# Kernel optimization log

Hardware: AMD Instinct MI355X
Metric: run time of the kernel (lower is better)

The kernel has to match this reference:

```python
import jax, jax.numpy as jnp
import numpy as np

B, S, HID = 2, 2048, 4096
NH, NKV, D = 32, 8, 128  # heads, kv heads, head_dim
GROUPS = NH // NKV
THETA = 10000.0


def _rope_tables():
    inv_freq = 1.0 / (THETA ** (np.arange(0, D, 2, dtype=np.float32) / D))
    pos = np.arange(S, dtype=np.float32)
    freqs = pos[:, None] * inv_freq[None, :]          # [S, D/2]
    emb = np.concatenate([freqs, freqs], axis=-1)      # [S, D]
    cos = np.broadcast_to(np.cos(emb)[None], (B, S, D)).copy()
    sin = np.broadcast_to(np.sin(emb)[None], (B, S, D)).copy()
    return jnp.asarray(cos), jnp.asarray(sin)


def setup_inputs() -> dict:
    key = jax.random.key(0)
    ks = jax.random.split(key, 5)
    hidden_states = jax.random.normal(ks[0], (B, S, HID), dtype=jnp.float32)
    cos, sin = _rope_tables()
    std = 0.02
    Wq = jax.random.normal(ks[1], (NH * D, HID), dtype=jnp.float32) * std
    Wk = jax.random.normal(ks[2], (NKV * D, HID), dtype=jnp.float32) * std
    Wv = jax.random.normal(ks[3], (NKV * D, HID), dtype=jnp.float32) * std
    Wo = jax.random.normal(ks[4], (HID, NH * D), dtype=jnp.float32) * std
    return {"hidden_states": hidden_states, "cos": cos, "sin": sin,
            "Wq": Wq, "Wk": Wk, "Wv": Wv, "Wo": Wo}


def _rotate_half(x):
    x1, x2 = jnp.split(x, 2, axis=-1)
    return jnp.concatenate([-x2, x1], axis=-1)


def reference(hidden_states, cos, sin, Wq, Wk, Wv, Wo):
    b, s, _ = hidden_states.shape
    # QKV projections (no bias; attention_bias=False)
    q = (hidden_states @ Wq.T).reshape(b, s, NH, D).transpose(0, 2, 1, 3)    # [B,NH,S,D]
    k = (hidden_states @ Wk.T).reshape(b, s, NKV, D).transpose(0, 2, 1, 3)   # [B,NKV,S,D]
    v = (hidden_states @ Wv.T).reshape(b, s, NKV, D).transpose(0, 2, 1, 3)
    # RoPE (HF apply_rotary_pos_emb: cos/sin unsqueezed at head dim)
    c = cos[:, None, :, :]
    sn = sin[:, None, :, :]
    q = q * c + _rotate_half(q) * sn
    k = k * c + _rotate_half(k) * sn
    # GQA repeat_kv
    k = jnp.repeat(k, GROUPS, axis=1)                                        # [B,NH,S,D]
    v = jnp.repeat(v, GROUPS, axis=1)
    # dense evalmode: scores + causal mask + fp32 softmax
    scores = jnp.einsum('bhqd,bhkd->bhqk', q, k) / jnp.sqrt(jnp.float32(D))
    causal = jnp.triu(jnp.ones((s, s), dtype=bool), k=1)                     # True above diag
    scores = jnp.where(causal[None, None], jnp.float32(-jnp.inf), scores)
    attn = jax.nn.softmax(scores.astype(jnp.float32), axis=-1).astype(v.dtype)
    out = jnp.einsum('bhqk,bhkd->bhqd', attn, v)                             # [B,NH,S,D]
    out = out.transpose(0, 2, 1, 3).reshape(b, s, NH * D)
    return out @ Wo.T
```

## Files before the change

### kernel.cpp

```cpp
#include <hip/hip_runtime.h>
#include <hip/hip_bf16.h>

#define DEV __device__ __forceinline__

typedef __attribute__((ext_vector_type(8))) short bf16x8;
typedef __attribute__((ext_vector_type(4))) short s16x4;
typedef __attribute__((ext_vector_type(4))) float f32x4;

constexpr int B_ = 2, S_ = 2048, HID_ = 4096, NH_ = 32, NKV_ = 8, D_ = 128;
constexpr int GROUPS_ = NH_ / NKV_;
constexpr float QSCALE_ = 0.08838834764831845f * 1.4426950408889634f;

DEV unsigned short f2bf(float x) {
    union { float f; unsigned int u; } v; v.f = x;
    unsigned int r = v.u + 0x7fffu + ((v.u >> 16) & 1u);
    return (unsigned short)(r >> 16);
}

DEV f32x4 mfma16(bf16x8 a, bf16x8 b, f32x4 c) {
    return __builtin_amdgcn_mfma_f32_16x16x32_bf16(a, b, c, 0, 0, 0);
}

DEV void gll16(const void* g, void* l) {
    __builtin_amdgcn_global_load_lds(
        (const __attribute__((address_space(1))) unsigned int*)g,
        (__attribute__((address_space(3))) unsigned int*)l, 16, 0, 0);
}

DEV int vperm(int s) {
    return (s & ~31) | (((s >> 2) & 3) << 3) | (((s >> 4) & 1) << 2) | (s & 3);
}

__global__ __launch_bounds__(256) void cast_all_k(
    const float* __restrict__ s0, const float* __restrict__ s1,
    const float* __restrict__ s2, const float* __restrict__ s3,
    const float* __restrict__ s4,
    unsigned short* __restrict__ d0, unsigned short* __restrict__ d1,
    unsigned short* __restrict__ d2, unsigned short* __restrict__ d3,
    unsigned short* __restrict__ d4)
{
    int bb = blockIdx.x;
    const float* s; unsigned short* d; int off;
    if      (bb < 8192)  { s = s0; d = d0; off = bb; }
    else if (bb < 16384) { s = s1; d = d1; off = bb - 8192; }
    else if (bb < 18432) { s = s2; d = d2; off = bb - 16384; }
    else if (bb < 20480) { s = s3; d = d3; off = bb - 18432; }
    else                 { s = s4; d = d4; off = bb - 20480; }
    size_t i = ((size_t)off * 256 + threadIdx.x) * 8;
    const f32x4* sp = (const f32x4*)(s + i);
    f32x4 a = sp[0], b = sp[1];
    bf16x8 o;
    o[0] = (short)f2bf(a[0]); o[1] = (short)f2bf(a[1]);
    o[2] = (short)f2bf(a[2]); o[3] = (short)f2bf(a[3]);
    o[4] = (short)f2bf(b[0]); o[5] = (short)f2bf(b[1]);
    o[6] = (short)f2bf(b[2]); o[7] = (short)f2bf(b[3]);
    *(bf16x8*)(d + i) = o;
}

template<int EPI>
__global__ __launch_bounds__(512, 2) void gemm256_k(
    const unsigned short* __restrict__ A, const unsigned short* __restrict__ Bw,
    float* __restrict__ Cf, unsigned short* __restrict__ Qo,
    const float* __restrict__ cosT, const float* __restrict__ sinT,
    int M, int N, int K)
{
    __shared__ __align__(16) unsigned short lds[65536];
    const int tid = threadIdx.x, lane = tid & 63;
    const int w = tid >> 6, wm = w >> 2, wn = w & 3;
    const int la = lane & 15, lb = lane >> 4;

    const int nwg = (int)gridDim.x;
    const int cpx = nwg >> 3;
    const int bid = (int)blockIdx.x;
    const int sw = (bid & 7) * cpx + (bid >> 3);
    const int ntn = N >> 8;
    const int bm = (sw / ntn) << 8, bn = (sw % ntn) << 8;

    const int srow = tid >> 3;
    const int scol8 = (tid & 7) ^ (srow & 7);
    const size_t rK = (size_t)K;
    const unsigned short* gA = A + (size_t)(bm + srow) * rK + scol8 * 8;
    const unsigned short* gB = Bw + (size_t)(bn + srow) * rK + scol8 * 8;

#define STAGE_A_H0(buf, kt) { gll16(gA + (size_t)(kt),            &lds[(buf)*16384 + tid*8]); \
                              gll16(gA + (size_t)(kt) + 128*rK,   &lds[(buf)*16384 + 8192 + tid*8]); }
#define STAGE_A_H1(buf, kt) { gll16(gA + (size_t)(kt) + 64*rK,    &lds[(buf)*16384 + 4096 + tid*8]); \
                              gll16(gA + (size_t)(kt) + 192*rK,   &lds[(buf)*16384 + 12288 + tid*8]); }
#define STAGE_B_H0(buf, kt) { gll16(gB + (size_t)(kt),            &lds[32768 + (buf)*16384 + tid*8]); \
                              gll16(gB + (size_t)(kt) + 64*rK,    &lds[32768 + (buf)*16384 + 4096 + tid*8]); }
#define STAGE_B_H1(buf, kt) { gll16(gB + (size_t)(kt) + 128*rK,   &lds[32768 + (buf)*16384 + 8192 + tid*8]); \
                              gll16(gB + (size_t)(kt) + 192*rK,   &lds[32768 + (buf)*16384 + 12288 + tid*8]); }
#define SB0() __builtin_amdgcn_sched_barrier(0)

    f32x4 acc[8][4];
#pragma unroll
    for (int m = 0; m < 8; ++m)
#pragma unroll
        for (int j = 0; j < 4; ++j) acc[m][j] = f32x4{0.f, 0.f, 0.f, 0.f};

    auto rdA = [&](int buf, int m, int kk) -> bf16x8 {
        int r = wm * 128 + m * 16 + la;
        int slot = (kk * 4 + lb) ^ (la & 7);
        return *(const bf16x8*)&lds[buf * 16384 + r * 64 + slot * 8];
    };
    auto rdB = [&](int buf, int j, int kk) -> bf16x8 {
        int r = (wn + 4 * j) * 16 + la;
        int slot = (kk * 4 + lb) ^ (la & 7);
        return *(const bf16x8*)&lds[32768 + buf * 16384 + r * 64 + slot * 8];
    };

    STAGE_A_H0(0, 0); STAGE_B_H0(0, 0); STAGE_B_H1(0, 0); STAGE_A_H1(0, 0);

    bf16x8 af[4][2], b01[2][2], b23[2][2];
    int cur = 0;
    const int nt = K >> 6;
    for (int t = 0; t < nt; ++t) {
        const bool pre = (t + 1 < nt);
        const int kn = (t + 1) << 6;
        const int nb = cur ^ 1;
        asm volatile("s_waitcnt vmcnt(2)" ::: "memory");
        SB0(); __builtin_amdgcn_s_barrier(); SB0();
#pragma unroll
        for (int m = 0; m < 4; ++m)
#pragma unroll
            for (int kk = 0; kk < 2; ++kk) af[m][kk] = rdA(cur, m, kk);
#pragma unroll
        for (int j = 0; j < 2; ++j)
#pragma unroll
            for (int kk = 0; kk < 2; ++kk) b01[j][kk] = rdB(cur, j, kk);
        if (pre) STAGE_A_H0(nb, kn);
        __builtin_amdgcn_s_setprio(1);
#pragma unroll
        for (int kk = 0; kk < 2; ++kk)
#pragma unroll
            for (int m = 0; m < 4; ++m)
#pragma unroll
                for (int j = 0; j < 2; ++j)
                    acc[m][j] = mfma16(af[m][kk], b01[j][kk], acc[m][j]);
        __builtin_amdgcn_s_setprio(0);
#pragma unroll
        for (int j = 0; j < 2; ++j)
#pragma unroll
            for (int kk = 0; kk < 2; ++kk) b23[j][kk] = rdB(cur, j + 2, kk);
        if (pre) STAGE_B_H0(nb, kn);
        __builtin_amdgcn_s_setprio(1);
#pragma unroll
        for (int kk = 0; kk < 2; ++kk)
#pragma unroll
            for (int m = 0; m < 4; ++m)
#pragma unroll
                for (int j = 0; j < 2; ++j)
                    acc[m][j + 2] = mfma16(af[m][kk], b23[j][kk], acc[m][j + 2]);
        __builtin_amdgcn_s_setprio(0);
        if (pre) { asm volatile("s_waitcnt vmcnt(4)" ::: "memory"); }
        else     { asm volatile("s_waitcnt vmcnt(0)" ::: "memory"); }
        SB0(); __builtin_amdgcn_s_barrier(); SB0();
#pragma unroll
        for (int m = 0; m < 4; ++m)
#pragma unroll
            for (int kk = 0; kk < 2; ++kk) af[m][kk] = rdA(cur, m + 4, kk);
        if (pre) STAGE_B_H1(nb, kn);
        __builtin_amdgcn_s_setprio(1);
#pragma unroll
        for (int kk = 0; kk < 2; ++kk)
#pragma unroll
            for (int m = 0; m < 4; ++m)
#pragma unroll
                for (int j = 0; j < 2; ++j)
                    acc[m + 4][j + 2] = mfma16(af[m][kk], b23[j][kk], acc[m + 4][j + 2]);
        __builtin_amdgcn_s_setprio(0);
        if (pre) STAGE_A_H1(nb, kn);
        __builtin_amdgcn_s_setprio(1);
#pragma unroll
        for (int kk = 0; kk < 2; ++kk)
#pragma unroll
            for (int m = 0; m < 4; ++m)
#pragma unroll
                for (int j = 0; j < 2; ++j)
                    acc[m + 4][j] = mfma16(af[m][kk], b01[j][kk], acc[m + 4][j]);
        __builtin_amdgcn_s_setprio(0);
        cur ^= 1;
    }
#undef STAGE_A_H0
#undef STAGE_A_H1
#undef STAGE_B_H0
#undef STAGE_B_H1

    const int srow0 = bm + wm * 128;
    if constexpr (EPI == 0) {
#pragma unroll
        for (int m = 0; m < 8; ++m)
#pragma unroll
            for (int j = 0; j < 4; ++j) {
                int col = bn + (wn + 4 * j) * 16 + la;
#pragma unroll
                for (int r = 0; r < 4; ++r)
                    Cf[(size_t)(srow0 + m * 16 + lb * 4 + r) * N + col] = acc[m][j][r];
            }
    } else {
        const int hbase = bn >> 7;
        const int d = wn * 16 + la;
#pragma unroll
        for (int m = 0; m < 8; ++m) {
#pragma unroll
            for (int r = 0; r < 4; ++r) {
                int row = srow0 + m * 16 + lb * 4 + r;
                float cv = cosT[(size_t)row * D_ + d];
                float sv = sinT[(size_t)row * D_ + d];
#pragma unroll
                for (int p = 0; p < 2; ++p) {
                    float x1 = acc[m][p * 2 + 0][r], x2 = acc[m][p * 2 + 1][r];
                    unsigned short* o = Qo + (size_t)row * (NH_ * D_) + (hbase + p) * D_ + d;
                    o[0]  = f2bf((x1 * cv - x2 * sv) * QSCALE_);
                    o[64] = f2bf((x2 * cv + x1 * sv) * QSCALE_);
                }
            }
        }
    }
}

__global__ __launch_bounds__(512, 4) void gemm_kv_k(
    const unsigned short* __restrict__ A, const unsigned short* __restrict__ Bw,
    unsigned short* __restrict__ Ko, unsigned short* __restrict__ Vo,
    const float* __restrict__ cosT, const float* __restrict__ sinT,
    int M, int K)
{
    __shared__ __align__(16) unsigned short lds[32768];
    const int tid = threadIdx.x, lane = tid & 63;
    const int w = tid >> 6, wm = w >> 2, wn = w & 3;
    const int la = lane & 15, lb = lane >> 4;

    const int nwg = (int)gridDim.x;
    const int cpx = nwg >> 3;
    const int bid = (int)blockIdx.x;
    const int sw = (bid & 7) * cpx + (bid >> 3);
    const int ntn = 2048 >> 7;
    const int bm = (sw / ntn) << 7, bn = (sw % ntn) << 7;

    const int srow = tid >> 3;
    const int scol8 = (tid & 7) ^ (srow & 7);
    const size_t rK = (size_t)K;
    const unsigned short* gA = A + (size_t)(bm + srow) * rK + scol8 * 8;
    const unsigned short* gB = Bw + (size_t)(bn + srow) * rK + scol8 * 8;

#define KV_STG_A(buf, kt)  { gll16(gA + (size_t)(kt),          &lds[(buf)*8192 + tid*8]); \
                             gll16(gA + (size_t)(kt) + 64*rK,  &lds[(buf)*8192 + 4096 + tid*8]); }
#define KV_STG_B0(buf, kt)   gll16(gB + (size_t)(kt),          &lds[16384 + (buf)*8192 + tid*8])
#define KV_STG_B1(buf, kt)   gll16(gB + (size_t)(kt) + 64*rK,  &lds[16384 + (buf)*8192 + 4096 + tid*8])
#define SB0() __builtin_amdgcn_sched_barrier(0)

    f32x4 acc[4][2];
#pragma unroll
    for (int m = 0; m < 4; ++m)
#pragma unroll
        for (int j = 0; j < 2; ++j) acc[m][j] = f32x4{0.f, 0.f, 0.f, 0.f};

    auto rdA = [&](int buf, int m, int kk) -> bf16x8 {
        int r = wm * 64 + m * 16 + la;
        int slot = (kk * 4 + lb) ^ (la & 7);
        return *(const bf16x8*)&lds[buf * 8192 + r * 64 + slot * 8];
    };
    auto rdB = [&](int buf, int j, int kk) -> bf16x8 {
        int r = (wn + 4 * j) * 16 + la;
        int slot = (kk * 4 + lb) ^ (la & 7);
        return *(const bf16x8*)&lds[16384 + buf * 8192 + r * 64 + slot * 8];
    };

    KV_STG_A(0, 0); KV_STG_B0(0, 0); KV_STG_B1(0, 0);

    bf16x8 af[4][2], bf0[2], bf1[2];
    int cur = 0;
    const int nt = K >> 6;
    for (int t = 0; t < nt; ++t) {
        const bool pre = (t + 1 < nt);
        const int kn = (t + 1) << 6;
        const int nb = cur ^ 1;
        asm volatile("s_waitcnt vmcnt(1)" ::: "memory");
        SB0(); __builtin_amdgcn_s_barrier(); SB0();
#pragma unroll
        for (int m = 0; m < 4; ++m)
#pragma unroll
            for (int kk = 0; kk < 2; ++kk) af[m][kk] = rdA(cur, m, kk);
#pragma unroll
        for (int kk = 0; kk < 2; ++kk) bf0[kk] = rdB(cur, 0, kk);
        if (pre) { KV_STG_A(nb, kn); KV_STG_B0(nb, kn); }
        __builtin_amdgcn_s_setprio(1);
#pragma unroll
        for (int kk = 0; kk < 2; ++kk)
#pragma unroll
            for (int m = 0; m < 4; ++m)
                acc[m][0] = mfma16(af[m][kk], bf0[kk], acc[m][0]);
        __builtin_amdgcn_s_setprio(0);
        if (pre) { asm volatile("s_waitcnt vmcnt(3)" ::: "memory"); }
        else     { asm volatile("s_waitcnt vmcnt(0)" ::: "memory"); }
        SB0(); __builtin_amdgcn_s_barrier(); SB0();
#pragma unroll
        for (int kk = 0; kk < 2; ++kk) bf1[kk] = rdB(cur, 1, kk);
        if (pre) KV_STG_B1(nb, kn);
        __builtin_amdgcn_s_setprio(1);
#pragma unroll
        for (int kk = 0; kk < 2; ++kk)
#pragma unroll
            for (int m = 0; m < 4; ++m)
                acc[m][1] = mfma16(af[m][kk], bf1[kk], acc[m][1]);
        __builtin_amdgcn_s_setprio(0);
        cur ^= 1;
    }
#undef KV_STG_A
#undef KV_STG_B0
#undef KV_STG_B1
#undef SB0

    const int rbase = bm + wm * 64;
    if (bn < 1024) {
        const int hbase = bn >> 7;
        const int d = wn * 16 + la;
#pragma unroll
        for (int m = 0; m < 4; ++m)
#pragma unroll
            for (int r = 0; r < 4; ++r) {
                int row = rbase + m * 16 + lb * 4 + r;
                float cv = cosT[(size_t)row * D_ + d];
                float sv = sinT[(size_t)row * D_ + d];
                float x1 = acc[m][0][r], x2 = acc[m][1][r];
                unsigned short* o = Ko + (size_t)row * (NKV_ * D_) + hbase * D_ + d;
                o[0]  = f2bf(x1 * cv - x2 * sv);
                o[64] = f2bf(x2 * cv + x1 * sv);
            }
    } else {
        const int kv = (bn - 1024) >> 7;
#pragma unroll
        for (int m = 0; m < 4; ++m) {
            int row = rbase + m * 16 + lb * 4;
            int b = row >> 11, s = row & (S_ - 1);
            int sp = vperm(s);
#pragma unroll
            for (int j = 0; j < 2; ++j) {
                int d = (wn + 4 * j) * 16 + la;
                s16x4 pk;
#pragma unroll
                for (int r = 0; r < 4; ++r) pk[r] = (short)f2bf(acc[m][j][r]);
                *(s16x4*)&Vo[((size_t)(b * NKV_ + kv) * D_ + d) * S_ + sp] = pk;
            }
        }
    }
}

template<int EPI, bool ABF16>
__global__ __launch_bounds__(256) void gemm_legacy_k(
    const void* __restrict__ Ap, const float* __restrict__ Bp,
    void* __restrict__ Cp, const float* __restrict__ cosT,
    const float* __restrict__ sinT, int M, int N, int K, float scale)
{
    constexpr int LDT = 40;
    __shared__ __align__(16) unsigned short Asm[128 * LDT];
    __shared__ __align__(16) unsigned short Bsm[128 * LDT];
    const int tid = threadIdx.x;
    const int lane = tid & 63;
    const int w = tid >> 6;
    const int la = lane & 15, lb = lane >> 4;
    const int ntn = N >> 7;
    const int bm = (int)(blockIdx.x / ntn) << 7;
    const int bn = (int)(blockIdx.x % ntn) << 7;

    f32x4 acc[2][8];
#pragma unroll
    for (int i = 0; i < 2; ++i)
#pragma unroll
        for (int j = 0; j < 8; ++j) acc[i][j] = f32x4{0.f, 0.f, 0.f, 0.f};

    for (int kt = 0; kt < K; kt += 32) {
        if constexpr (!ABF16) {
#pragma unroll
            for (int it = 0; it < 4; ++it) {
                int idx = it * 256 + tid;
                int r = idx >> 3, c = (idx & 7) << 2;
                const float* g = (const float*)Ap + (size_t)(bm + r) * K + kt + c;
                f32x4 v = *(const f32x4*)g;
                union { unsigned long long q; unsigned short u[4]; } pk;
                pk.u[0] = f2bf(v[0]); pk.u[1] = f2bf(v[1]);
                pk.u[2] = f2bf(v[2]); pk.u[3] = f2bf(v[3]);
                *(unsigned long long*)&Asm[r * LDT + c] = pk.q;
            }
        } else {
#pragma unroll
            for (int it = 0; it < 2; ++it) {
                int idx = it * 256 + tid;
                int r = idx >> 2, c = (idx & 3) << 3;
                const unsigned short* g =
                    (const unsigned short*)Ap + (size_t)(bm + r) * K + kt + c;
                *(bf16x8*)&Asm[r * LDT + c] = *(const bf16x8*)g;
            }
        }
#pragma unroll
        for (int it = 0; it < 4; ++it) {
            int idx = it * 256 + tid;
            int r = idx >> 3, c = (idx & 7) << 2;
            const float* g = Bp + (size_t)(bn + r) * K + kt + c;
            f32x4 v = *(const f32x4*)g;
            union { unsigned long long q; unsigned short u[4]; } pk;
            pk.u[0] = f2bf(v[0]); pk.u[1] = f2bf(v[1]);
            pk.u[2] = f2bf(v[2]); pk.u[3] = f2bf(v[3]);
            *(unsigned long long*)&Bsm[r * LDT + c] = pk.q;
        }
        __syncthreads();
        bf16x8 af0 = *(bf16x8*)&Asm[(w * 32 + la) * LDT + lb * 8];
        bf16x8 af1 = *(bf16x8*)&Asm[(w * 32 + 16 + la) * LDT + lb * 8];
#pragma unroll
        for (int nb = 0; nb < 8; ++nb) {
            bf16x8 bfr = *(bf16x8*)&Bsm[(nb * 16 + la) * LDT + lb * 8];
            acc[0][nb] = mfma16(af0, bfr, acc[0][nb]);
            acc[1][nb] = mfma16(af1, bfr, acc[1][nb]);
        }
        __syncthreads();
    }

    const int rbase = bm + w * 32;
    if constexpr (EPI == 0) {
        float* C = (float*)Cp;
#pragma unroll
        for (int mf = 0; mf < 2; ++mf)
#pragma unroll
            for (int nb = 0; nb < 8; ++nb)
#pragma unroll
                for (int r = 0; r < 4; ++r)
                    C[(size_t)(rbase + mf * 16 + lb * 4 + r) * N + bn + nb * 16 + la] =
                        acc[mf][nb][r];
    } else if constexpr (EPI == 1) {
        unsigned short* C = (unsigned short*)Cp;
#pragma unroll
        for (int mf = 0; mf < 2; ++mf) {
#pragma unroll
            for (int r = 0; r < 4; ++r) {
                int m = rbase + mf * 16 + lb * 4 + r;
                const float* cb = cosT + (size_t)m * D_;
                const float* sb = sinT + (size_t)m * D_;
#pragma unroll
                for (int nb = 0; nb < 4; ++nb) {
                    int d = nb * 16 + la;
                    float c = cb[d], s = sb[d];
                    float x1 = acc[mf][nb][r], x2 = acc[mf][nb + 4][r];
                    C[(size_t)m * N + bn + d]      = f2bf((x1 * c - x2 * s) * scale);
                    C[(size_t)m * N + bn + d + 64] = f2bf((x2 * c + x1 * s) * scale);
                }
            }
        }
    } else {
        unsigned short* C = (unsigned short*)Cp;
#pragma unroll
        for (int mf = 0; mf < 2; ++mf)
#pragma unroll
            for (int nb = 0; nb < 8; ++nb)
#pragma unroll
                for (int r = 0; r < 4; ++r) {
                    int m = rbase + mf * 16 + lb * 4 + r;
                    int b = m >> 11, s = m & (S_ - 1);
                    int n = bn + nb * 16 + la;
                    int kv = n >> 7, d = n & 127;
                    C[(((size_t)b * NKV_ + kv) * D_ + d) * S_ + vperm(s)] =
                        f2bf(acc[mf][nb][r]);
                }
    }
}

__global__ __launch_bounds__(256, 2) void attn5_k(
    const unsigned short* __restrict__ Qw,
    const unsigned short* __restrict__ Kw,
    const unsigned short* __restrict__ Vt,
    unsigned short* __restrict__ Ow)
{
    __shared__ __align__(16) unsigned short Ksm[2][64 * 128];
    __shared__ __align__(16) unsigned short Vsm[2][128 * 64];
    const int tid = threadIdx.x, lane = tid & 63, w = tid >> 6;
    const int la = lane & 15, lb = lane >> 4;
    const int blk = blockIdx.x;
    const int qbi = (S_ / 128 - 1) - (blk >> 6);
    const int bh = blk & 63;
    const int b = bh >> 5, h = bh & 31;
    const int kvh = h >> 2;
    const int qb = qbi * 128;
    const int qw0 = qb + w * 32;

    bf16x8 fq[2][4];
    const unsigned short* qp =
        Qw + ((size_t)(b * S_ + qw0 + la) * NH_ + h) * D_ + lb * 8;
#pragma unroll
    for (int mq = 0; mq < 2; ++mq)
#pragma unroll
        for (int kc = 0; kc < 4; ++kc)
            fq[mq][kc] = *(const bf16x8*)(qp + (size_t)mq * 16 * NH_ * D_ + kc * 32);

    bf16x8 ones;
#pragma unroll
    for (int i = 0; i < 8; ++i) ones[i] = (short)0x3F80;

    float m_[2];
    f32x4 oacc[8][2], lacc[2];
    m_[0] = m_[1] = -__builtin_inff();
    lacc[0] = lacc[1] = f32x4{0.f, 0.f, 0.f, 0.f};
#pragma unroll
    for (int db = 0; db < 8; ++db)
#pragma unroll
        for (int mq = 0; mq < 2; ++mq) oacc[db][mq] = f32x4{0.f, 0.f, 0.f, 0.f};

    const int krb = tid >> 4, ksl = tid & 15;
    const int vrb = tid >> 3, vsl = tid & 7;
    const unsigned short* kbase = Kw + ((size_t)b * S_ * NKV_ + kvh) * D_;
    const unsigned short* vbase = Vt + ((size_t)(b * NKV_ + kvh) * D_) * S_;

#define STAGE_KV(buf, kv0) {                                                   \
    _Pragma("unroll")                                                          \
    for (int it = 0; it < 4; ++it) {                                           \
        int row = it * 16 + krb;                                               \
        int cc = ksl ^ (row & 7);                                              \
        gll16(kbase + (size_t)(kv0 + row) * NKV_ * D_ + cc * 8,                \
              &Ksm[buf][(it * 256 + tid) * 8]);                                \
    }                                                                          \
    _Pragma("unroll")                                                          \
    for (int it = 0; it < 4; ++it) {                                           \
        int row = it * 32 + vrb;                                               \
        int cc = vsl ^ (row & 7);                                              \
        gll16(vbase + (size_t)row * S_ + (kv0) + cc * 8,                       \
              &Vsm[buf][(it * 256 + tid) * 8]);                                \
    }                                                                          \
}
#define SB0() __builtin_amdgcn_sched_barrier(0)

    STAGE_KV(0, 0);
    int cur = 0;
    const int ntiles = (qb + 128) >> 6;
    for (int t = 0; t < ntiles; ++t) {
        const int kv0 = t << 6;
        const bool pre = (t + 1 < ntiles);
        if (pre) STAGE_KV(cur ^ 1, kv0 + 64);
        if (pre) { asm volatile("s_waitcnt vmcnt(8)" ::: "memory"); }
        else     { asm volatile("s_waitcnt vmcnt(0)" ::: "memory"); }
        SB0(); __builtin_amdgcn_s_barrier(); SB0();

        if (kv0 < qw0 + 32) {
            f32x4 sacc[4][2];
#pragma unroll
            for (int nk = 0; nk < 4; ++nk)
#pragma unroll
                for (int mq = 0; mq < 2; ++mq) sacc[nk][mq] = f32x4{0.f, 0.f, 0.f, 0.f};
#pragma unroll
            for (int kc = 0; kc < 4; ++kc) {
#pragma unroll
                for (int nk = 0; nk < 4; ++nk) {
                    int row = nk * 16 + la;
                    int slot = (kc * 4 + lb) ^ (la & 7);
                    bf16x8 fk = *(const bf16x8*)&Ksm[cur][row * 128 + slot * 8];
#pragma unroll
                    for (int mq = 0; mq < 2; ++mq)
                        sacc[nk][mq] = mfma16(fk, fq[mq][kc], sacc[nk][mq]);
                }
            }
            const bool diag = (kv0 + 63 > qw0);
            float pv[4][2][4];
            float pm[2];
#pragma unroll
            for (int mq = 0; mq < 2; ++mq) {
                int q = qw0 + mq * 16 + la;
                float mx = -__builtin_inff();
#pragma unroll
                for (int nk = 0; nk < 4; ++nk)
#pragma unroll
                    for (int r = 0; r < 4; ++r) {
                        float s = sacc[nk][mq][r];
                        if (diag) {
                            int k = kv0 + nk * 16 + lb * 4 + r;
                            s = (k <= q) ? s : -__builtin_inff();
                        }
                        pv[nk][mq][r] = s;
                        mx = fmaxf(mx, s);
                    }
                mx = fmaxf(mx, __shfl_xor(mx, 16));
                mx = fmaxf(mx, __shfl_xor(mx, 32));
                pm[mq] = mx;
            }
            const bool upd =
                __any((pm[0] > m_[0] + 8.f) || (pm[1] > m_[1] + 8.f));
            if (upd) {
#pragma unroll
                for (int mq = 0; mq < 2; ++mq) {
                    float mn = fmaxf(m_[mq], pm[mq]);
                    float fac = exp2f(m_[mq] - mn);
                    m_[mq] = mn;
                    lacc[mq] *= fac;
#pragma unroll
                    for (int db = 0; db < 8; ++db) oacc[db][mq] *= fac;
                }
            }
#pragma unroll
            for (int nk = 0; nk < 4; ++nk)
#pragma unroll
                for (int mq = 0; mq < 2; ++mq)
#pragma unroll
                    for (int r = 0; r < 4; ++r)
                        pv[nk][mq][r] = exp2f(pv[nk][mq][r] - m_[mq]);
            union { bf16x8 v; __hip_bfloat162 h[4]; } fp[2][2];
#pragma unroll
            for (int mq = 0; mq < 2; ++mq)
#pragma unroll
                for (int ks = 0; ks < 2; ++ks) {
                    fp[mq][ks].h[0] = __float22bfloat162_rn(
                        float2{pv[2 * ks][mq][0], pv[2 * ks][mq][1]});
                    fp[mq][ks].h[1] = __float22bfloat162_rn(
                        float2{pv[2 * ks][mq][2], pv[2 * ks][mq][3]});
                    fp[mq][ks].h[2] = __float22bfloat162_rn(
                        float2{pv[2 * ks + 1][mq][0], pv[2 * ks + 1][mq][1]});
                    fp[mq][ks].h[3] = __float22bfloat162_rn(
                        float2{pv[2 * ks + 1][mq][2], pv[2 * ks + 1][mq][3]});
                }
#pragma unroll
            for (int ks = 0; ks < 2; ++ks) {
#pragma unroll
                for (int db = 0; db < 8; ++db) {
                    int row = db * 16 + la;
                    int slot = (ks * 4 + lb) ^ (row & 7);
                    bf16x8 fv = *(const bf16x8*)&Vsm[cur][row * 64 + slot * 8];
#pragma unroll
                    for (int mq = 0; mq < 2; ++mq)
                        oacc[db][mq] = mfma16(fv, fp[mq][ks].v, oacc[db][mq]);
                }
#pragma unroll
                for (int mq = 0; mq < 2; ++mq)
                    lacc[mq] = mfma16(ones, fp[mq][ks].v, lacc[mq]);
            }
        }
        SB0(); __builtin_amdgcn_s_barrier(); SB0();
        cur ^= 1;
    }
#undef STAGE_KV
#undef SB0

#pragma unroll
    for (int mq = 0; mq < 2; ++mq) {
        float rl = 1.f / lacc[mq][0];
        int q = qw0 + mq * 16 + la;
#pragma unroll
        for (int db = 0; db < 8; ++db) {
            f32x4 o = oacc[db][mq];
            s16x4 pk;
#pragma unroll
            for (int r = 0; r < 4; ++r) pk[r] = (short)f2bf(o[r] * rl);
            int d = db * 16 + lb * 4;
            *(s16x4*)(Ow + (size_t)(b * S_ + q) * (NH_ * D_) + h * D_ + d) = pk;
        }
    }
}

extern "C" void kernel_launch(void* const* d_in, const int* in_sizes, int n_in,
                              void* d_out, int out_size, void* d_ws, size_t ws_size,
                              hipStream_t stream) {
    const float* hs   = (const float*)d_in[0];
    const float* cosT = (const float*)d_in[1];
    const float* sinT = (const float*)d_in[2];
    const float* Wq   = (const float*)d_in[3];
    const float* Wk   = (const float*)d_in[4];
    const float* Wv   = (const float*)d_in[5];
    const float* Wo   = (const float*)d_in[6];

    constexpr size_t Qn  = (size_t)B_ * S_ * NH_ * D_;
    constexpr size_t Kn  = (size_t)B_ * S_ * NKV_ * D_;
    constexpr size_t Hn  = (size_t)B_ * S_ * HID_;
    constexpr size_t Wqn = (size_t)NH_ * D_ * HID_;
    constexpr size_t Wkn = (size_t)NKV_ * D_ * HID_;

    unsigned short* Qws   = (unsigned short*)d_ws;
    unsigned short* Kws   = Qws + Qn;
    unsigned short* Vtws  = Kws + Kn;
    unsigned short* AOws  = Vtws + Kn;
    unsigned short* hsb   = AOws + Qn;
    unsigned short* Wqkvb = hsb + Hn;
    unsigned short* Wob   = Wqkvb + Wqn + 2 * Wkn;
    constexpr size_t need = (Qn + 2 * Kn + Qn + Hn + Wqn + 2 * Wkn + Wqn) * 2;

    const int M = B_ * S_;
    dim3 blk(256);

    if (ws_size >= need) {
        cast_all_k<<<dim3(28672), blk, 0, stream>>>(
            hs, Wq, Wk, Wv, Wo,
            hsb, Wqkvb, Wqkvb + Wqn, Wqkvb + Wqn + Wkn, Wob);

        gemm256_k<1><<<dim3((M / 256) * (HID_ / 256)), dim3(512), 0, stream>>>(
            hsb, Wqkvb, nullptr, Qws, cosT, sinT, M, HID_, HID_);
        gemm_kv_k<<<dim3((M / 128) * (2048 / 128)), dim3(512), 0, stream>>>(
            hsb, Wqkvb + Wqn, Kws, Vtws, cosT, sinT, M, HID_);
        attn5_k<<<dim3(B_ * NH_ * (S_ / 128)), blk, 0, stream>>>(
            Qws, Kws, Vtws, AOws);
        gemm256_k<0><<<dim3((M / 256) * (HID_ / 256)), dim3(512), 0, stream>>>(
            AOws, Wob, (float*)d_out, nullptr, nullptr, nullptr, M, HID_, NH_ * D_);
    } else {
        unsigned short* Qf = (unsigned short*)d_ws;
        unsigned short* Kf = Qf + Qn;
        unsigned short* Vf = Kf + Kn;
        unsigned short* AOf = Vf + Kn;
        gemm_legacy_k<1, false><<<dim3((M / 128) * (NH_ * D_ / 128)), blk, 0, stream>>>(
            hs, Wq, Qf, cosT, sinT, M, NH_ * D_, HID_, QSCALE_);
        gemm_legacy_k<1, false><<<dim3((M / 128) * (NKV_ * D_ / 128)), blk, 0, stream>>>(
            hs, Wk, Kf, cosT, sinT, M, NKV_ * D_, HID_, 1.0f);
        gemm_legacy_k<3, false><<<dim3((M / 128) * (NKV_ * D_ / 128)), blk, 0, stream>>>(
            hs, Wv, Vf, nullptr, nullptr, M, NKV_ * D_, HID_, 0.f);
        attn5_k<<<dim3(B_ * NH_ * (S_ / 128)), blk, 0, stream>>>(
            Qf, Kf, Vf, AOf);
        gemm_legacy_k<0, true><<<dim3((M / 128) * (HID_ / 128)), blk, 0, stream>>>(
            AOf, Wo, (float*)d_out, nullptr, nullptr, M, HID_, NH_ * D_, 0.f);
    }
}
```

Measured before the change: 452.6 us.

## Halve attention KV tile to 32 keys for higher occupancy and reorder query blocks

The attention kernel now processes 32-key tiles instead of 64, halving the LDS footprint and the score/probability register arrays. Launch bounds go from 2 to 4 blocks per CU, and the V tile layout and fragment indexing are rebuilt so one MFMA k-step covers the 32 keys. Query-block scheduling changes from strictly longest-first to the 8 longest blocks followed by the shortest ones ascending, which alters load balance. The trade is twice as many barriers and tile iterations, plus possible register spills under the tighter launch bound.

```diff
diff --git a/kernel.cpp b/kernel.cpp
--- a/kernel.cpp
+++ b/kernel.cpp
@@ -463,18 +463,19 @@
     }
 }
 
-__global__ __launch_bounds__(256, 2) void attn5_k(
+__global__ __launch_bounds__(256, 4) void attn7_k(
     const unsigned short* __restrict__ Qw,
     const unsigned short* __restrict__ Kw,
     const unsigned short* __restrict__ Vt,
     unsigned short* __restrict__ Ow)
 {
-    __shared__ __align__(16) unsigned short Ksm[2][64 * 128];
-    __shared__ __align__(16) unsigned short Vsm[2][128 * 64];
+    __shared__ __align__(16) unsigned short Ksm[2][32 * 128];
+    __shared__ __align__(16) unsigned short Vsm[2][64 * 64];
     const int tid = threadIdx.x, lane = tid & 63, w = tid >> 6;
     const int la = lane & 15, lb = lane >> 4;
     const int blk = blockIdx.x;
-    const int qbi = (S_ / 128 - 1) - (blk >> 6);
+    const int g = blk >> 6;
+    const int qbi = (g < 8) ? (15 - g) : (g - 8);
     const int bh = blk & 63;
     const int b = bh >> 5, h = bh & 31;
     const int kvh = h >> 2;
@@ -510,17 +511,18 @@
 
 #define STAGE_KV(buf, kv0) {                                                   \
     _Pragma("unroll")                                                          \
-    for (int it = 0; it < 4; ++it) {                                           \
+    for (int it = 0; it < 2; ++it) {                                           \
         int row = it * 16 + krb;                                               \
         int cc = ksl ^ (row & 7);                                              \
         gll16(kbase + (size_t)(kv0 + row) * NKV_ * D_ + cc * 8,                \
               &Ksm[buf][(it * 256 + tid) * 8]);                                \
     }                                                                          \
     _Pragma("unroll")                                                          \
-    for (int it = 0; it < 4; ++it) {                                           \
+    for (int it = 0; it < 2; ++it) {                                           \
         int row = it * 32 + vrb;                                               \
         int cc = vsl ^ (row & 7);                                              \
-        gll16(vbase + (size_t)row * S_ + (kv0) + cc * 8,                       \
+        int dg = ((cc >> 2) << 6) + row;                                       \
+        gll16(vbase + (size_t)dg * S_ + (kv0) + (cc & 3) * 8,                  \
               &Vsm[buf][(it * 256 + tid) * 8]);                                \
     }                                                                          \
 }
@@ -528,25 +530,25 @@
 
     STAGE_KV(0, 0);
     int cur = 0;
-    const int ntiles = (qb + 128) >> 6;
+    const int ntiles = (qb + 128) >> 5;
     for (int t = 0; t < ntiles; ++t) {
-        const int kv0 = t << 6;
+        const int kv0 = t << 5;
         const bool pre = (t + 1 < ntiles);
-        if (pre) STAGE_KV(cur ^ 1, kv0 + 64);
-        if (pre) { asm volatile("s_waitcnt vmcnt(8)" ::: "memory"); }
+        if (pre) STAGE_KV(cur ^ 1, kv0 + 32);
+        if (pre) { asm volatile("s_waitcnt vmcnt(4)" ::: "memory"); }
         else     { asm volatile("s_waitcnt vmcnt(0)" ::: "memory"); }
         SB0(); __builtin_amdgcn_s_barrier(); SB0();
 
         if (kv0 < qw0 + 32) {
-            f32x4 sacc[4][2];
-#pragma unroll
-            for (int nk = 0; nk < 4; ++nk)
+            f32x4 sacc[2][2];
+#pragma unroll
+            for (int nk = 0; nk < 2; ++nk)
 #pragma unroll
                 for (int mq = 0; mq < 2; ++mq) sacc[nk][mq] = f32x4{0.f, 0.f, 0.f, 0.f};
 #pragma unroll
             for (int kc = 0; kc < 4; ++kc) {
 #pragma unroll
-                for (int nk = 0; nk < 4; ++nk) {
+                for (int nk = 0; nk < 2; ++nk) {
                     int row = nk * 16 + la;
                     int slot = (kc * 4 + lb) ^ (la & 7);
                     bf16x8 fk = *(const bf16x8*)&Ksm[cur][row * 128 + slot * 8];
@@ -555,15 +557,15 @@
                         sacc[nk][mq] = mfma16(fk, fq[mq][kc], sacc[nk][mq]);
                 }
             }
-            const bool diag = (kv0 + 63 > qw0);
-            float pv[4][2][4];
+            const bool diag = (kv0 + 31 > qw0);
+            float pv[2][2][4];
             float pm[2];
 #pragma unroll
             for (int mq = 0; mq < 2; ++mq) {
                 int q = qw0 + mq * 16 + la;
                 float mx = -__builtin_inff();
 #pragma unroll
-                for (int nk = 0; nk < 4; ++nk)
+                for (int nk = 0; nk < 2; ++nk)
 #pragma unroll
                     for (int r = 0; r < 4; ++r) {
                         float s = sacc[nk][mq][r];
@@ -592,41 +594,36 @@
                 }
             }
 #pragma unroll
-            for (int nk = 0; nk < 4; ++nk)
+            for (int nk = 0; nk < 2; ++nk)
 #pragma unroll
                 for (int mq = 0; mq < 2; ++mq)
 #pragma unroll
                     for (int r = 0; r < 4; ++r)
                         pv[nk][mq][r] = exp2f(pv[nk][mq][r] - m_[mq]);
-            union { bf16x8 v; __hip_bfloat162 h[4]; } fp[2][2];
+            union { bf16x8 v; __hip_bfloat162 h[4]; } fp[2];
+#pragma unroll
+            for (int mq = 0; mq < 2; ++mq) {
+                fp[mq].h[0] = __float22bfloat162_rn(
+                    float2{pv[0][mq][0], pv[0][mq][1]});
+                fp[mq].h[1] = __float22bfloat162_rn(
+                    float2{pv[0][mq][2], pv[0][mq][3]});
+                fp[mq].h[2] = __float22bfloat162_rn(
+                    float2{pv[1][mq][0], pv[1][mq][1]});
+                fp[mq].h[3] = __float22bfloat162_rn(
+                    float2{pv[1][mq][2], pv[1][mq][3]});
+            }
+#pragma unroll
+            for (int db = 0; db < 8; ++db) {
+                int r64 = (db & 3) * 16 + la;
+                int slot = (((db >> 2) << 2) + lb) ^ (r64 & 7);
+                bf16x8 fv = *(const bf16x8*)&Vsm[cur][r64 * 64 + slot * 8];
+#pragma unroll
+                for (int mq = 0; mq < 2; ++mq)
+                    oacc[db][mq] = mfma16(fv, fp[mq].v, oacc[db][mq]);
+            }
 #pragma unroll
             for (int mq = 0; mq < 2; ++mq)
-#pragma unroll
-                for (int ks = 0; ks < 2; ++ks) {
-                    fp[mq][ks].h[0] = __float22bfloat162_rn(
-                        float2{pv[2 * ks][mq][0], pv[2 * ks][mq][1]});
-                    fp[mq][ks].h[1] = __float22bfloat162_rn(
-                        float2{pv[2 * ks][mq][2], pv[2 * ks][mq][3]});
-                    fp[mq][ks].h[2] = __float22bfloat162_rn(
-                        float2{pv[2 * ks + 1][mq][0], pv[2 * ks + 1][mq][1]});
-                    fp[mq][ks].h[3] = __float22bfloat162_rn(
-                        float2{pv[2 * ks + 1][mq][2], pv[2 * ks + 1][mq][3]});
-                }
-#pragma unroll
-            for (int ks = 0; ks < 2; ++ks) {
-#pragma unroll
-                for (int db = 0; db < 8; ++db) {
-                    int row = db * 16 + la;
-                    int slot = (ks * 4 + lb) ^ (row & 7);
-                    bf16x8 fv = *(const bf16x8*)&Vsm[cur][row * 64 + slot * 8];
-#pragma unroll
-                    for (int mq = 0; mq < 2; ++mq)
-                        oacc[db][mq] = mfma16(fv, fp[mq][ks].v, oacc[db][mq]);
-                }
-#pragma unroll
-                for (int mq = 0; mq < 2; ++mq)
-                    lacc[mq] = mfma16(ones, fp[mq][ks].v, lacc[mq]);
-            }
+                lacc[mq] = mfma16(ones, fp[mq].v, lacc[mq]);
         }
         SB0(); __builtin_amdgcn_s_barrier(); SB0();
         cur ^= 1;
@@ -688,7 +685,7 @@
             hsb, Wqkvb, nullptr, Qws, cosT, sinT, M, HID_, HID_);
         gemm_kv_k<<<dim3((M / 128) * (2048 / 128)), dim3(512), 0, stream>>>(
             hsb, Wqkvb + Wqn, Kws, Vtws, cosT, sinT, M, HID_);
-        attn5_k<<<dim3(B_ * NH_ * (S_ / 128)), blk, 0, stream>>>(
+        attn7_k<<<dim3(B_ * NH_ * (S_ / 128)), blk, 0, stream>>>(
             Qws, Kws, Vtws, AOws);
         gemm256_k<0><<<dim3((M / 256) * (HID_ / 256)), dim3(512), 0, stream>>>(
             AOws, Wob, (float*)d_out, nullptr, nullptr, nullptr, M, HID_, NH_ * D_);
@@ -703,7 +700,7 @@
             hs, Wk, Kf, cosT, sinT, M, NKV_ * D_, HID_, 1.0f);
         gemm_legacy_k<3, false><<<dim3((M / 128) * (NKV_ * D_ / 128)), blk, 0, stream>>>(
             hs, Wv, Vf, nullptr, nullptr, M, NKV_ * D_, HID_, 0.f);
-        attn5_k<<<dim3(B_ * NH_ * (S_ / 128)), blk, 0, stream>>>(
+        attn7_k<<<dim3(B_ * NH_ * (S_ / 128)), blk, 0, stream>>>(
             Qf, Kf, Vf, AOf);
         gemm_legacy_k<0, true><<<dim3((M / 128) * (HID_ / 128)), blk, 0, stream>>>(
             AOf, Wo, (float*)d_out, nullptr, nullptr, M, HID_, NH_ * D_, 0.f);
```

After: 594.1 us. +31.2%, slower.
